# Performance work log

Measured on AMD Instinct MI355X. Metric: run time of the kernel, lower is better.

## Reference

```python
import jax, jax.numpy as jnp
import numpy as np

D_MODEL = 1024
NUM_HEADS = 16
D_K = D_MODEL // NUM_HEADS
WINDOW = 256


def setup_inputs() -> dict:
    key = jax.random.key(0)
    ks = jax.random.split(key, 11)
    B, S, D = 2, 2048, D_MODEL
    scale = 1.0 / np.sqrt(D)
    inp = {
        "q": jax.random.normal(ks[0], (B, S, D), jnp.float32),
        "k": jax.random.normal(ks[1], (B, S, D), jnp.float32),
        "v": jax.random.normal(ks[2], (B, S, D), jnp.float32),
        "Wq": jax.random.normal(ks[3], (D, D), jnp.float32) * scale,
        "bq": jnp.zeros((D,), jnp.float32),
        "Wk": jax.random.normal(ks[4], (D, D), jnp.float32) * scale,
        "bk": jnp.zeros((D,), jnp.float32),
        "Wv": jax.random.normal(ks[5], (D, D), jnp.float32) * scale,
        "bv": jnp.zeros((D,), jnp.float32),
        "Wo": jax.random.normal(ks[6], (D, D), jnp.float32) * scale,
        "bo": jnp.zeros((D,), jnp.float32),
    }
    return inp


def _split_heads(x):
    B, S, _ = x.shape
    return x.reshape(B, S, NUM_HEADS, D_K).transpose(0, 2, 1, 3)  # [B,H,S,d_k]


def reference(q, k, v, Wq, bq, Wk, bk, Wv, bv, Wo, bo):
    B, S, D = q.shape
    qh = _split_heads(q @ Wq + bq)
    kh = _split_heads(k @ Wk + bk)
    vh = _split_heads(v @ Wv + bv)

    # dense scores then sliding-window band mask (|i-j| <= WINDOW), as in SparseAttention
    scores = jnp.einsum("bhqd,bhkd->bhqk", qh, kh) / jnp.sqrt(jnp.float32(D_K))
    idx = jnp.arange(S)
    band = jnp.abs(idx[:, None] - idx[None, :]) <= WINDOW  # [S,S]
    scores = jnp.where(band[None, None], scores, -jnp.inf)
    attn = jax.nn.softmax(scores, axis=-1)

    out = jnp.einsum("bhqk,bhkd->bhqd", attn, vh)
    out = out.transpose(0, 2, 1, 3).reshape(B, S, D)  # combine heads
    out = out @ Wo + bo
    return out, attn
```

## Files before the change

### kernel.cpp

```cpp
#include <hip/hip_runtime.h>


constexpr int Bb = 2, Ss = 2048, Dd = 1024, Hh = 16, WINw = 256;
constexpr size_t XS_SLAB = (size_t)4096 * 2048;
constexpr size_t WT_SLAB = (size_t)1024 * 2048;
constexpr size_t QB_SLAB = (size_t)4096 * 1024;

typedef short s16x8 __attribute__((ext_vector_type(8)));
typedef float f32x4 __attribute__((ext_vector_type(4)));

__device__ inline unsigned short f2bf(float x) {
  unsigned u = __float_as_uint(x);
  u += 0x7fff + ((u >> 16) & 1);
  return (unsigned short)(u >> 16);
}
__device__ inline float bf2f(unsigned short h) {
  return __uint_as_float(((unsigned)h) << 16);
}

__global__ __launch_bounds__(256) void convert_x(
    const float* __restrict__ x0, const float* __restrict__ x1,
    const float* __restrict__ x2, unsigned short* __restrict__ Xs) {
  int z = blockIdx.z;
  const float* src = z == 0 ? x0 : (z == 1 ? x1 : x2);
  unsigned short* dst = Xs + (size_t)z * XS_SLAB;
  size_t idx = ((size_t)blockIdx.x * 256 + threadIdx.x) * 4;
  int r = (int)(idx >> 10);
  int c = (int)(idx & 1023);
  f32x4 v = *(const f32x4*)&src[idx];
  unsigned short hi[4], lo[4];
#pragma unroll
  for (int i = 0; i < 4; ++i) {
    float vi = v[i];
    hi[i] = f2bf(vi);
    lo[i] = f2bf(vi - bf2f(hi[i]));
  }
  ushort4 h4 = {hi[0], hi[1], hi[2], hi[3]};
  ushort4 l4 = {lo[0], lo[1], lo[2], lo[3]};
  *(ushort4*)&dst[(size_t)r * 2048 + c] = h4;
  *(ushort4*)&dst[(size_t)r * 2048 + 1024 + c] = l4;
}

__global__ __launch_bounds__(256) void convert_w(
    const float* __restrict__ w0, const float* __restrict__ w1,
    const float* __restrict__ w2, const float* __restrict__ w3,
    unsigned short* __restrict__ Wt) {
  __shared__ float T[64][65];
  int z = blockIdx.z;
  const float* W = z == 0 ? w0 : (z == 1 ? w1 : (z == 2 ? w2 : w3));
  unsigned short* dst = Wt + (size_t)z * WT_SLAB;
  int k0 = blockIdx.y * 64, n0 = blockIdx.x * 64;
  int t = threadIdx.x;
#pragma unroll
  for (int i = 0; i < 4; ++i) {
    int row = (t >> 4) + i * 16;
    int c4 = (t & 15) * 4;
    f32x4 v = *(const f32x4*)&W[(size_t)(k0 + row) * 1024 + n0 + c4];
    T[row][c4 + 0] = v[0]; T[row][c4 + 1] = v[1];
    T[row][c4 + 2] = v[2]; T[row][c4 + 3] = v[3];
  }
  __syncthreads();
  int n = t >> 2;
  int kc = (t & 3) * 16;
  unsigned short hi[16], lo[16];
#pragma unroll
  for (int j = 0; j < 16; ++j) {
    float x = T[kc + j][n];
    hi[j] = f2bf(x);
    lo[j] = f2bf(x - bf2f(hi[j]));
  }
  size_t base = (size_t)(n0 + n) * 2048 + k0 + kc;
#pragma unroll
  for (int j4 = 0; j4 < 4; ++j4) {
    ushort4 h4 = {hi[j4 * 4], hi[j4 * 4 + 1], hi[j4 * 4 + 2], hi[j4 * 4 + 3]};
    ushort4 l4 = {lo[j4 * 4], lo[j4 * 4 + 1], lo[j4 * 4 + 2], lo[j4 * 4 + 3]};
    *(ushort4*)&dst[base + j4 * 4] = h4;
    *(ushort4*)&dst[base + 1024 + j4 * 4] = l4;
  }
}

template <int F32OUT>
__global__ __launch_bounds__(256) void gemm_bf16x3(
    const unsigned short* __restrict__ Abase,
    const unsigned short* __restrict__ Wtbase, void* __restrict__ Cbase,
    const float* __restrict__ bb0, const float* __restrict__ bb1,
    const float* __restrict__ bb2) {
  __shared__ s16x8 As[512];
  __shared__ s16x8 Bs[512];
  int z = blockIdx.z;
  const unsigned short* A = Abase + (size_t)z * XS_SLAB;
  const unsigned short* Wt = Wtbase + (size_t)z * WT_SLAB;
  const float* bias = z == 0 ? bb0 : (z == 1 ? bb1 : bb2);
  const float scl = (!F32OUT && z == 0) ? 0.125f : 1.0f;

  const int t = threadIdx.x;
  const int lane = t & 63, wave = t >> 6;
  const int wm = wave & 1, wn = wave >> 1;
  const int bm = blockIdx.y * 128, bn = blockIdx.x * 128;

  f32x4 acc[4][4] = {};

  const int s0 = t, s1 = t + 256;
  const int r0 = s0 >> 2, c0 = (s0 & 3) ^ ((r0 >> 1) & 3);
  const int r1 = s1 >> 2, c1 = (s1 & 3) ^ ((r1 >> 1) & 3);
  const unsigned short* A0 = A + (size_t)(bm + r0) * 2048 + c0 * 8;
  const unsigned short* A1 = A + (size_t)(bm + r1) * 2048 + c1 * 8;
  const unsigned short* B0 = Wt + (size_t)(bn + r0) * 2048 + c0 * 8;
  const unsigned short* B1 = Wt + (size_t)(bn + r1) * 2048 + c1 * 8;

  s16x8 va0 = *(const s16x8*)(A0);
  s16x8 va1 = *(const s16x8*)(A1);
  s16x8 vb0 = *(const s16x8*)(B0);
  s16x8 vb1 = *(const s16x8*)(B1);

  const int m15 = lane & 15, q = lane >> 4;

  for (int kb = 0; kb < 3072; kb += 32) {
    __syncthreads();
    As[s0] = va0; As[s1] = va1;
    Bs[s0] = vb0; Bs[s1] = vb1;
    __syncthreads();

    int kb2 = kb + 32;
    if (kb2 >= 3072) kb2 = 0;
    int asrc = kb2 < 1024 ? kb2 : kb2 - 1024;
    int wsrc = kb2 < 2048 ? kb2 : kb2 - 2048;
    va0 = *(const s16x8*)(A0 + asrc);
    va1 = *(const s16x8*)(A1 + asrc);
    vb0 = *(const s16x8*)(B0 + wsrc);
    vb1 = *(const s16x8*)(B1 + wsrc);

    s16x8 af[4], bf[4];
#pragma unroll
    for (int mt = 0; mt < 4; ++mt) {
      int r = wm * 64 + mt * 16 + m15;
      af[mt] = As[r * 4 + (q ^ ((r >> 1) & 3))];
    }
#pragma unroll
    for (int nt = 0; nt < 4; ++nt) {
      int r = wn * 64 + nt * 16 + m15;
      bf[nt] = Bs[r * 4 + (q ^ ((r >> 1) & 3))];
    }
#pragma unroll
    for (int mt = 0; mt < 4; ++mt)
#pragma unroll
      for (int nt = 0; nt < 4; ++nt)
        acc[mt][nt] = __builtin_amdgcn_mfma_f32_16x16x32_bf16(
            af[mt], bf[nt], acc[mt][nt], 0, 0, 0);
  }

#pragma unroll
  for (int nt = 0; nt < 4; ++nt) {
    int col = bn + wn * 64 + nt * 16 + m15;
    float bv = bias[col];
#pragma unroll
    for (int mt = 0; mt < 4; ++mt) {
      int rowb = bm + wm * 64 + mt * 16 + q * 4;
#pragma unroll
      for (int i = 0; i < 4; ++i) {
        float val = (acc[mt][nt][i] + bv) * scl;
        if (F32OUT) {
          ((float*)Cbase)[(size_t)(rowb + i) * 1024 + col] = val;
        } else {
          ((unsigned short*)Cbase + (size_t)z * QB_SLAB)
              [(size_t)(rowb + i) * 1024 + col] = f2bf(val);
        }
      }
    }
  }
}

__global__ __launch_bounds__(256) void transpose_v(
    const unsigned short* __restrict__ Vb, unsigned short* __restrict__ Vt) {
  __shared__ unsigned short T[64][88];
  const int b = blockIdx.z, h = blockIdx.y, s0 = blockIdx.x * 64;
  const int t = threadIdx.x;
  {
    int row = t >> 2, part = t & 3;
    const unsigned short* src =
        Vb + (size_t)(b * Ss + s0 + row) * 1024 + h * 64 + part * 16;
    s16x8 v0 = *(const s16x8*)src;
    s16x8 v1 = *(const s16x8*)(src + 8);
    *(s16x8*)&T[row][part * 16] = v0;
    *(s16x8*)&T[row][part * 16 + 8] = v1;
  }
  __syncthreads();
  {
    int d = t & 63, sw = t >> 6;
    unsigned short tmp[16];
#pragma unroll
    for (int i = 0; i < 16; ++i) tmp[i] = T[sw * 16 + i][d];
    unsigned short* dst =
        Vt + ((size_t)((b * Hh + h) * 64 + d)) * 2048 + s0 + sw * 16;
    *(s16x8*)dst = *(const s16x8*)&tmp[0];
    *(s16x8*)(dst + 8) = *(const s16x8*)&tmp[8];
  }
}

constexpr int SW3 = 556;
__global__ __launch_bounds__(256) void attn_v3(
    const unsigned short* __restrict__ Qb, const unsigned short* __restrict__ Kb,
    const unsigned short* __restrict__ Vt, float* __restrict__ attn,
    unsigned short* __restrict__ XsAO) {
  __shared__ float P[16 * SW3];
  const int t = threadIdx.x;
  const int lane = t & 63, wave = t >> 6;
  const int m15 = lane & 15, quad = lane >> 4;
  const int bid = blockIdx.x;
  const int qt = bid & 127, h = (bid >> 7) & 15, b = bid >> 11;
  const int q0 = qt * 16;
  int jlo = q0 - WINw; if (jlo < 0) jlo = 0;
  int jhi = q0 + 15 + WINw; if (jhi > Ss - 1) jhi = Ss - 1;
  const int ncols = jhi - jlo + 1;
  const int ntiles = ncols >> 4;

  {
    const unsigned short* qrow =
        Qb + (size_t)(b * Ss + q0 + m15) * 1024 + h * 64 + quad * 8;
    s16x8 aq0 = *(const s16x8*)qrow;
    s16x8 aq1 = *(const s16x8*)(qrow + 32);
    for (int nt = wave; nt < ntiles; nt += 4) {
      const unsigned short* krow =
          Kb + (size_t)(b * Ss + jlo + nt * 16 + m15) * 1024 + h * 64 + quad * 8;
      s16x8 b0 = *(const s16x8*)krow;
      s16x8 b1 = *(const s16x8*)(krow + 32);
      f32x4 c = {0.f, 0.f, 0.f, 0.f};
      c = __builtin_amdgcn_mfma_f32_16x16x32_bf16(aq0, b0, c, 0, 0, 0);
      c = __builtin_amdgcn_mfma_f32_16x16x32_bf16(aq1, b1, c, 0, 0, 0);
      float* pp = &P[(quad * 4) * SW3 + nt * 16 + m15];
#pragma unroll
      for (int i = 0; i < 4; ++i) pp[i * SW3] = c[i];
    }
  }
  __syncthreads();

  {
#pragma unroll
    for (int ri = 0; ri < 4; ++ri) {
      const int r = wave * 4 + ri;
      const int qq = q0 + r;
      int lo = qq - WINw; if (lo < 0) lo = 0;
      int hi = qq + WINw; if (hi > Ss - 1) hi = Ss - 1;
      const int clo = lo - jlo, chi = hi - jlo;
      float sv[9];
      bool ib[9];
      float m = -1e30f;
#pragma unroll
      for (int k2 = 0; k2 < 9; ++k2) {
        int c = k2 * 64 + lane;
        bool inb = (c >= clo) && (c <= chi);
        ib[k2] = inb;
        float vv = inb ? P[r * SW3 + c] : -1e30f;
        sv[k2] = vv;
        m = fmaxf(m, vv);
      }
#pragma unroll
      for (int off = 32; off; off >>= 1) m = fmaxf(m, __shfl_xor(m, off, 64));
      float e[9], l = 0.f;
#pragma unroll
      for (int k2 = 0; k2 < 9; ++k2) { e[k2] = __expf(sv[k2] - m); l += e[k2]; }
#pragma unroll
      for (int off = 32; off; off >>= 1) l += __shfl_xor(l, off, 64);
      const float inv = 1.f / l;
#pragma unroll
      for (int k2 = 0; k2 < 9; ++k2) {
        int c = k2 * 64 + lane;
        if (c < 544) P[r * SW3 + c] = ib[k2] ? e[k2] * inv : 0.f;
      }
      float* arow = attn + ((size_t)((b * Hh + h) * Ss + qq)) * Ss;
#pragma unroll
      for (int i = 0; i < 8; ++i) {
        int col = i * 256 + lane * 4;
        int c = col - jlo;
        f32x4 v = {0.f, 0.f, 0.f, 0.f};
        if (c >= 0 && c <= 540) v = *(const f32x4*)&P[r * SW3 + c];
        *(f32x4*)&arow[col] = v;
      }
    }
  }
  __syncthreads();

  {
    const int ntk = (ncols + 31) >> 5;
    const unsigned short* vtrow =
        Vt + ((size_t)((b * Hh + h) * 64 + wave * 16 + m15)) * 2048 + jlo +
        quad * 8;
    f32x4 o = {0.f, 0.f, 0.f, 0.f};
    for (int ks = 0; ks < ntk; ++ks) {
      const float* pa = &P[m15 * SW3 + ks * 32 + quad * 8];
      f32x4 p0 = *(const f32x4*)pa;
      f32x4 p1 = *(const f32x4*)(pa + 4);
      s16x8 af;
#pragma unroll
      for (int i = 0; i < 4; ++i) af[i] = (short)f2bf(p0[i]);
#pragma unroll
      for (int i = 0; i < 4; ++i) af[4 + i] = (short)f2bf(p1[i]);
      s16x8 bf = *(const s16x8*)(vtrow + ks * 32);
      o = __builtin_amdgcn_mfma_f32_16x16x32_bf16(af, bf, o, 0, 0, 0);
    }
    const int dcol = h * 64 + wave * 16 + m15;
#pragma unroll
    for (int i = 0; i < 4; ++i) {
      int row = q0 + quad * 4 + i;
      unsigned short hi = f2bf(o[i]);
      unsigned short lo = f2bf(o[i] - bf2f(hi));
      unsigned short* dst = XsAO + (size_t)(b * Ss + row) * 2048 + dcol;
      dst[0] = hi;
      dst[1024] = lo;
    }
  }
}

extern "C" void kernel_launch(void* const* d_in, const int* in_sizes, int n_in,
                              void* d_out, int out_size, void* d_ws,
                              size_t ws_size, hipStream_t stream) {
  const float* q  = (const float*)d_in[0];
  const float* k  = (const float*)d_in[1];
  const float* v  = (const float*)d_in[2];
  const float* Wq = (const float*)d_in[3];
  const float* bq = (const float*)d_in[4];
  const float* Wk = (const float*)d_in[5];
  const float* bk = (const float*)d_in[6];
  const float* Wv = (const float*)d_in[7];
  const float* bv = (const float*)d_in[8];
  const float* Wo = (const float*)d_in[9];
  const float* bo = (const float*)d_in[10];

  float* out = (float*)d_out;
  float* attn = out + (size_t)Bb * Ss * Dd;

  unsigned short* Xs   = (unsigned short*)d_ws;
  unsigned short* XsAO = Xs + 3 * XS_SLAB;
  unsigned short* Wt   = XsAO + XS_SLAB;
  unsigned short* Qb   = Wt + 4 * WT_SLAB;
  unsigned short* Kb   = Qb + QB_SLAB;
  unsigned short* Vb   = Kb + QB_SLAB;
  unsigned short* Vt   = Vb + QB_SLAB;

  hipLaunchKernelGGL(convert_x, dim3(4096, 1, 3), dim3(256), 0, stream,
                     q, k, v, Xs);
  hipLaunchKernelGGL(convert_w, dim3(16, 16, 4), dim3(256), 0, stream,
                     Wq, Wk, Wv, Wo, Wt);
  hipLaunchKernelGGL((gemm_bf16x3<0>), dim3(8, 32, 3), dim3(256), 0, stream,
                     Xs, Wt, (void*)Qb, bq, bk, bv);
  hipLaunchKernelGGL(transpose_v, dim3(32, 16, 2), dim3(256), 0, stream,
                     Vb, Vt);
  hipLaunchKernelGGL(attn_v3, dim3(Bb * Hh * (Ss / 16)), dim3(256), 0, stream,
                     Qb, Kb, Vt, attn, XsAO);
  hipLaunchKernelGGL((gemm_bf16x3<1>), dim3(8, 32, 1), dim3(256), 0, stream,
                     XsAO, Wt + 3 * WT_SLAB, (void*)out, bo, bo, bo);
}
```

Baseline: 820.8 us.

## Double-buffer GEMM tiles via direct global-to-LDS loads and use nontemporal stores

The bf16x3 GEMM now stages A and W tiles straight from global memory into LDS with global_load_lds into a two-slot buffer. The next tile is prefetched while MFMAs run on the current one, which removes the register round-trip and one barrier per k-step. Launch bounds ask for 3 blocks per CU. The output projection and the large attention-matrix writes now use nontemporal stores to limit cache pollution. A risk is that the wave*64 LDS destination layout must match the swizzled thread-to-slot mapping the old code used; if it does not, results will be wrong.

```diff
diff --git a/kernel.cpp b/kernel.cpp
--- a/kernel.cpp
+++ b/kernel.cpp
@@ -8,6 +8,13 @@
 
 typedef short s16x8 __attribute__((ext_vector_type(8)));
 typedef float f32x4 __attribute__((ext_vector_type(4)));
+
+typedef __attribute__((address_space(3))) unsigned int lds_uint;
+typedef const __attribute__((address_space(1))) unsigned int gbl_uint;
+
+__device__ __forceinline__ void gld_lds16(const void* g, void* l) {
+  __builtin_amdgcn_global_load_lds((gbl_uint*)g, (lds_uint*)l, 16, 0, 0);
+}
 
 __device__ inline unsigned short f2bf(float x) {
   unsigned u = __float_as_uint(x);
@@ -80,13 +87,13 @@
 }
 
 template <int F32OUT>
-__global__ __launch_bounds__(256) void gemm_bf16x3(
+__global__ __launch_bounds__(256, 3) void gemm_bf16x3(
     const unsigned short* __restrict__ Abase,
     const unsigned short* __restrict__ Wtbase, void* __restrict__ Cbase,
     const float* __restrict__ bb0, const float* __restrict__ bb1,
     const float* __restrict__ bb2) {
-  __shared__ s16x8 As[512];
-  __shared__ s16x8 Bs[512];
+  __shared__ s16x8 As[2][512];
+  __shared__ s16x8 Bs[2][512];
   int z = blockIdx.z;
   const unsigned short* A = Abase + (size_t)z * XS_SLAB;
   const unsigned short* Wt = Wtbase + (size_t)z * WT_SLAB;
@@ -108,38 +115,36 @@
   const unsigned short* B0 = Wt + (size_t)(bn + r0) * 2048 + c0 * 8;
   const unsigned short* B1 = Wt + (size_t)(bn + r1) * 2048 + c1 * 8;
 
-  s16x8 va0 = *(const s16x8*)(A0);
-  s16x8 va1 = *(const s16x8*)(A1);
-  s16x8 vb0 = *(const s16x8*)(B0);
-  s16x8 vb1 = *(const s16x8*)(B1);
-
   const int m15 = lane & 15, q = lane >> 4;
 
+  gld_lds16(A0, &As[0][wave * 64]);
+  gld_lds16(A1, &As[0][256 + wave * 64]);
+  gld_lds16(B0, &Bs[0][wave * 64]);
+  gld_lds16(B1, &Bs[0][256 + wave * 64]);
+  __syncthreads();
+
+  int cur = 0;
   for (int kb = 0; kb < 3072; kb += 32) {
-    __syncthreads();
-    As[s0] = va0; As[s1] = va1;
-    Bs[s0] = vb0; Bs[s1] = vb1;
-    __syncthreads();
-
-    int kb2 = kb + 32;
-    if (kb2 >= 3072) kb2 = 0;
-    int asrc = kb2 < 1024 ? kb2 : kb2 - 1024;
-    int wsrc = kb2 < 2048 ? kb2 : kb2 - 2048;
-    va0 = *(const s16x8*)(A0 + asrc);
-    va1 = *(const s16x8*)(A1 + asrc);
-    vb0 = *(const s16x8*)(B0 + wsrc);
-    vb1 = *(const s16x8*)(B1 + wsrc);
+    const int kn = kb + 32;
+    if (kn < 3072) {
+      int asrc = kn < 1024 ? kn : kn - 1024;
+      int wsrc = kn < 2048 ? kn : kn - 2048;
+      gld_lds16(A0 + asrc, &As[cur ^ 1][wave * 64]);
+      gld_lds16(A1 + asrc, &As[cur ^ 1][256 + wave * 64]);
+      gld_lds16(B0 + wsrc, &Bs[cur ^ 1][wave * 64]);
+      gld_lds16(B1 + wsrc, &Bs[cur ^ 1][256 + wave * 64]);
+    }
 
     s16x8 af[4], bf[4];
 #pragma unroll
     for (int mt = 0; mt < 4; ++mt) {
       int r = wm * 64 + mt * 16 + m15;
-      af[mt] = As[r * 4 + (q ^ ((r >> 1) & 3))];
+      af[mt] = As[cur][r * 4 + (q ^ ((r >> 1) & 3))];
     }
 #pragma unroll
     for (int nt = 0; nt < 4; ++nt) {
       int r = wn * 64 + nt * 16 + m15;
-      bf[nt] = Bs[r * 4 + (q ^ ((r >> 1) & 3))];
+      bf[nt] = Bs[cur][r * 4 + (q ^ ((r >> 1) & 3))];
     }
 #pragma unroll
     for (int mt = 0; mt < 4; ++mt)
@@ -147,6 +152,11 @@
       for (int nt = 0; nt < 4; ++nt)
         acc[mt][nt] = __builtin_amdgcn_mfma_f32_16x16x32_bf16(
             af[mt], bf[nt], acc[mt][nt], 0, 0, 0);
+
+    if (kn < 3072) {
+      __syncthreads();
+      cur ^= 1;
+    }
   }
 
 #pragma unroll
@@ -160,7 +170,8 @@
       for (int i = 0; i < 4; ++i) {
         float val = (acc[mt][nt][i] + bv) * scl;
         if (F32OUT) {
-          ((float*)Cbase)[(size_t)(rowb + i) * 1024 + col] = val;
+          __builtin_nontemporal_store(
+              val, &((float*)Cbase)[(size_t)(rowb + i) * 1024 + col]);
         } else {
           ((unsigned short*)Cbase + (size_t)z * QB_SLAB)
               [(size_t)(rowb + i) * 1024 + col] = f2bf(val);
@@ -274,7 +285,7 @@
         int c = col - jlo;
         f32x4 v = {0.f, 0.f, 0.f, 0.f};
         if (c >= 0 && c <= 540) v = *(const f32x4*)&P[r * SW3 + c];
-        *(f32x4*)&arow[col] = v;
+        __builtin_nontemporal_store(v, (f32x4*)&arow[col]);
       }
     }
   }
```

Measured after the change: 787.0 us. 4.1% less time.
